# Optimization experiments

Hardware: AMD Instinct MI355X
Metric: run time of the kernel (lower is better)

## Reference

```python
import jax, jax.numpy as jnp
from jax import lax
import numpy as np

H_SIZE = 1024      # max(hidden_size_list)
EXPAND = 2
INTER = EXPAND * H_SIZE            # 2048 intermediate size
NHEADS = 32                        # max(num_heads_list)
HEAD_DIM = INTER // NHEADS         # 64
NSTATE = 128                       # ssm state size
NGROUPS = 1
KCONV = 4                          # conv kernel
CHUNK = 256                        # chunk size for SSD scan
EPS = 1e-5                         # layer_norm_epsilon
CONV_DIM = INTER + 2 * NGROUPS * NSTATE        # 2304
PROJ_DIM = 2 * INTER + 2 * NGROUPS * NSTATE + NHEADS  # 4352


def setup_inputs() -> dict:
    key = jax.random.key(0)
    ks = jax.random.split(key, 9)
    B, S = 2, 4096
    return {
        "hidden_states": jax.random.normal(ks[0], (B, S, H_SIZE), jnp.float32),
        "in_proj_w": jax.random.normal(ks[1], (PROJ_DIM, H_SIZE), jnp.float32) * 0.02,
        "conv_w": jax.random.normal(ks[2], (CONV_DIM, 1, KCONV), jnp.float32) * 0.2,
        "conv_b": jax.random.normal(ks[3], (CONV_DIM,), jnp.float32) * 0.02,
        "dt_bias": jax.random.normal(ks[4], (NHEADS,), jnp.float32) * 0.1,
        "A_log": jax.random.uniform(ks[5], (NHEADS,), jnp.float32, 0.0, 1.0),
        "D": jax.random.normal(ks[6], (NHEADS,), jnp.float32),
        "norm_w": jnp.ones((INTER,), jnp.float32) + 0.01 * jax.random.normal(ks[7], (INTER,), jnp.float32),
        "out_proj_w": jax.random.normal(ks[8], (H_SIZE, INTER), jnp.float32) * 0.02,
    }


def _segsum(a):
    # a: [B,H,C,L] -> lower-triangular segment sums [B,H,C,L,L]
    L = a.shape[-1]
    cs = jnp.cumsum(a, axis=-1)
    ss = cs[..., :, None] - cs[..., None, :]
    mask = jnp.tril(jnp.ones((L, L), dtype=bool))
    return jnp.where(mask, ss, -jnp.inf)


def reference(hidden_states, in_proj_w, conv_w, conv_b, dt_bias, A_log, D, norm_w, out_proj_w):
    B, S, _ = hidden_states.shape
    proj = hidden_states @ in_proj_w.T                       # [B,S,4352]
    gate = proj[..., :INTER]                                 # [B,S,2048]
    hBC = proj[..., INTER:INTER + CONV_DIM]                  # [B,S,2304]
    dt = proj[..., INTER + CONV_DIM:]                        # [B,S,H]

    # causal depthwise conv1d + SiLU
    xc_ = jnp.transpose(hBC, (0, 2, 1))                      # [B,C,S]
    xc_ = lax.conv_general_dilated(xc_, conv_w, (1,), [(KCONV - 1, 0)],
                                   dimension_numbers=('NCH', 'OIH', 'NCH'),
                                   feature_group_count=CONV_DIM)
    xc_ = jax.nn.silu(xc_ + conv_b[None, :, None])
    hBC = jnp.transpose(xc_, (0, 2, 1))                      # [B,S,2304]

    h = hBC[..., :INTER]
    Bm = hBC[..., INTER:INTER + NGROUPS * NSTATE]
    Cm = hBC[..., INTER + NGROUPS * NSTATE:]

    dt = jax.nn.softplus(dt + dt_bias)                       # [B,S,H]
    dt = jnp.clip(dt, 0.0, None)                             # time_step_limit (0, inf)
    A = -jnp.exp(A_log)                                      # [H]

    NC = S // CHUNK
    xh = h.reshape(B, NC, CHUNK, NHEADS, HEAD_DIM)
    Bh = jnp.repeat(Bm.reshape(B, NC, CHUNK, NGROUPS, NSTATE), NHEADS // NGROUPS, axis=3)
    Ch = jnp.repeat(Cm.reshape(B, NC, CHUNK, NGROUPS, NSTATE), NHEADS // NGROUPS, axis=3)
    dtc = dt.reshape(B, NC, CHUNK, NHEADS)

    a = jnp.transpose(dtc * A, (0, 3, 1, 2))                 # [B,H,NC,L]
    A_cum = jnp.cumsum(a, axis=-1)                           # [B,H,NC,L]
    Lmat = jnp.exp(_segsum(a))                               # [B,H,NC,L,L]
    xdt = xh * dtc[..., None]                                # [B,NC,L,H,P]

    # intra-chunk (diagonal block) output
    Yd = jnp.einsum('bclhn,bcshn,bhcls,bcshp->bclhp', Ch, Bh, Lmat, xdt)

    # per-chunk final states
    decay = jnp.exp(A_cum[..., -1:] - A_cum)                 # [B,H,NC,L]
    states = jnp.einsum('bclhn,bhcl,bclhp->bchpn', Bh, decay, xdt)  # [B,NC,H,P,N]

    # inter-chunk recurrence over chunks
    g = jnp.exp(A_cum[..., -1])                              # [B,H,NC]
    def step(carry, inp):
        s_c, g_c = inp
        return carry * g_c[..., None, None] + s_c, carry
    _, prev = lax.scan(step, jnp.zeros((B, NHEADS, HEAD_DIM, NSTATE), states.dtype),
                       (jnp.moveaxis(states, 1, 0), jnp.moveaxis(g, 2, 0)))
    prev = jnp.moveaxis(prev, 0, 1)                          # [B,NC,H,P,N] state entering each chunk

    Yo = jnp.einsum('bclhn,bchpn,bhcl->bclhp', Ch, prev, jnp.exp(A_cum))

    y = (Yd + Yo + D[None, None, None, :, None] * xh).reshape(B, S, INTER)

    # gated RMSNorm (fp32 internally)
    yf = y.astype(jnp.float32) * jax.nn.silu(gate.astype(jnp.float32))
    var = jnp.mean(yf * yf, axis=-1, keepdims=True)
    y = norm_w * (yf * lax.rsqrt(var + EPS))

    return y @ out_proj_w.T
```

## Files before the change

### kernel.cpp

```cpp
#include <hip/hip_runtime.h>
#include <hip/hip_bf16.h>
#include <math.h>

#define H_SIZE   1024
#define INTER    2048
#define NHEADS   32
#define HEAD_DIM 64
#define NSTATE   128
#define KCONV    4
#define CHUNK    256
#define CONV_DIM (INTER + 2*NSTATE)
#define CIN_DIM  (CONV_DIM + NHEADS)
#define PROJ_DIM (2*INTER + 2*NSTATE + NHEADS)
#define BATCH    2
#define SEQ      4096
#define NC       (SEQ/CHUNK)
#define EPS_F    1e-5f

typedef __attribute__((ext_vector_type(8))) short bf16x8;
typedef __attribute__((ext_vector_type(4))) float f32x4;
typedef unsigned short ushort_t;

__device__ __forceinline__ ushort_t f2bf(float x) {
  unsigned u = __float_as_uint(x);
  u += 0x7fffu + ((u >> 16) & 1u);
  return (ushort_t)(u >> 16);
}
__device__ __forceinline__ float bf2f(ushort_t h) {
  return __uint_as_float((unsigned)h << 16);
}

__global__ __launch_bounds__(256) void convert_hl_kernel(
    const float* __restrict__ x, ushort_t* __restrict__ hi,
    ushort_t* __restrict__ lo, int n4) {
  int idx = blockIdx.x * 256 + threadIdx.x;
  int stride = gridDim.x * 256;
  for (int i = idx; i < n4; i += stride) {
    const float* p = x + (size_t)i * 4;
    float v0 = p[0], v1 = p[1], v2 = p[2], v3 = p[3];
    ushort_t h0 = f2bf(v0), h1 = f2bf(v1), h2 = f2bf(v2), h3 = f2bf(v3);
    ushort_t l0 = f2bf(v0 - bf2f(h0));
    ushort_t l1 = f2bf(v1 - bf2f(h1));
    ushort_t l2 = f2bf(v2 - bf2f(h2));
    ushort_t l3 = f2bf(v3 - bf2f(h3));
    *(uint2*)(hi + (size_t)i * 4) =
        make_uint2((unsigned)h0 | ((unsigned)h1 << 16), (unsigned)h2 | ((unsigned)h3 << 16));
    *(uint2*)(lo + (size_t)i * 4) =
        make_uint2((unsigned)l0 | ((unsigned)l1 << 16), (unsigned)l2 | ((unsigned)l3 << 16));
  }
}

__global__ __launch_bounds__(256) void convert_bc_kernel(
    const float* __restrict__ hbc, ushort_t* __restrict__ Bph,
    ushort_t* __restrict__ Bpl, ushort_t* __restrict__ Cph,
    ushort_t* __restrict__ Cpl) {
  const int n4 = (BATCH*SEQ) * 64;
  int idx = blockIdx.x * 256 + threadIdx.x;
  int stride = gridDim.x * 256;
  for (int i = idx; i < n4; i += stride) {
    int row = i >> 6;
    int c4 = (i & 63) * 4;
    float4 v = *(const float4*)(hbc + (size_t)row*CONV_DIM + INTER + c4);
    ushort_t h0 = f2bf(v.x), h1 = f2bf(v.y), h2 = f2bf(v.z), h3 = f2bf(v.w);
    ushort_t l0 = f2bf(v.x - bf2f(h0)), l1 = f2bf(v.y - bf2f(h1));
    ushort_t l2 = f2bf(v.z - bf2f(h2)), l3 = f2bf(v.w - bf2f(h3));
    uint2 hp = make_uint2((unsigned)h0 | ((unsigned)h1 << 16), (unsigned)h2 | ((unsigned)h3 << 16));
    uint2 lp = make_uint2((unsigned)l0 | ((unsigned)l1 << 16), (unsigned)l2 | ((unsigned)l3 << 16));
    if (c4 < 128) {
      *(uint2*)(Bph + (size_t)row*128 + c4) = hp;
      *(uint2*)(Bpl + (size_t)row*128 + c4) = lp;
    } else {
      *(uint2*)(Cph + (size_t)row*128 + (c4 - 128)) = hp;
      *(uint2*)(Cpl + (size_t)row*128 + (c4 - 128)) = lp;
    }
  }
}

#define LROW 40
template<int PLANES>
__global__ __launch_bounds__(256) void gemm_hl_mfma_kernel(
    const ushort_t* __restrict__ Ahi, const ushort_t* __restrict__ Alo,
    const ushort_t* __restrict__ Whi, const ushort_t* __restrict__ Wlo,
    float* __restrict__ C, int M, int N, int K, int nx) {
  __shared__ __align__(16) ushort_t Ah[128*LROW];
  __shared__ __align__(16) ushort_t Al[(PLANES==3) ? 128*LROW : 8];
  __shared__ __align__(16) ushort_t Wh[128*LROW], Wl[128*LROW];
  const int tid = threadIdx.x;
  const int lane = tid & 63, wid = tid >> 6;
  const int wr = wid >> 1, wc = wid & 1;
  const int fr = lane & 15, fg = lane >> 4;

  const int cpx = gridDim.x >> 3;
  const int logical = (blockIdx.x & 7) * cpx + (blockIdx.x >> 3);
  const int grp = logical / (nx * 4);
  const int rem = logical - grp * (nx * 4);
  const int bx = rem >> 2;
  const int by = grp * 4 + (rem & 3);
  const int m0 = by * 128, n0 = bx * 128;

  const int r0 = tid >> 2;
  const int kseg = (tid & 3) * 8;
  const int r1 = r0 + 64;
  const size_t a0 = (size_t)(m0 + r0) * K + kseg;
  const size_t a1 = (size_t)(m0 + r1) * K + kseg;
  const size_t w0 = (size_t)(n0 + r0) * K + kseg;
  const size_t w1 = (size_t)(n0 + r1) * K + kseg;
  const bool wv0 = (n0 + r0) < N, wv1 = (n0 + r1) < N;

  bf16x8 gA0, gA1, gAl0, gAl1, gW0, gW1, gWl0, gWl1;
  const bf16x8 z8 = {};
  f32x4 acc[4][4] = {};

  auto glod = [&](int k0) {
    gA0  = *(const bf16x8*)(Ahi + a0 + k0);
    gA1  = *(const bf16x8*)(Ahi + a1 + k0);
    if constexpr (PLANES == 3) {
      gAl0 = *(const bf16x8*)(Alo + a0 + k0);
      gAl1 = *(const bf16x8*)(Alo + a1 + k0);
    }
    gW0  = wv0 ? *(const bf16x8*)(Whi + w0 + k0) : z8;
    gW1  = wv1 ? *(const bf16x8*)(Whi + w1 + k0) : z8;
    gWl0 = wv0 ? *(const bf16x8*)(Wlo + w0 + k0) : z8;
    gWl1 = wv1 ? *(const bf16x8*)(Wlo + w1 + k0) : z8;
  };

  glod(0);
  for (int k0 = 0; k0 < K; k0 += 32) {
    __syncthreads();
    *(bf16x8*)&Ah[r0*LROW + kseg] = gA0;
    *(bf16x8*)&Ah[r1*LROW + kseg] = gA1;
    if constexpr (PLANES == 3) {
      *(bf16x8*)&Al[r0*LROW + kseg] = gAl0;
      *(bf16x8*)&Al[r1*LROW + kseg] = gAl1;
    }
    *(bf16x8*)&Wh[r0*LROW + kseg] = gW0;
    *(bf16x8*)&Wh[r1*LROW + kseg] = gW1;
    *(bf16x8*)&Wl[r0*LROW + kseg] = gWl0;
    *(bf16x8*)&Wl[r1*LROW + kseg] = gWl1;
    __syncthreads();
    if (k0 + 32 < K) glod(k0 + 32);

    bf16x8 wh[4], wl[4];
#pragma unroll
    for (int nf = 0; nf < 4; ++nf) {
      int off = (wc*64 + nf*16 + fr) * LROW + 8*fg;
      wh[nf] = *(const bf16x8*)&Wh[off];
      wl[nf] = *(const bf16x8*)&Wl[off];
    }
#pragma unroll
    for (int mf = 0; mf < 4; ++mf) {
      int aoff = (wr*64 + mf*16 + fr) * LROW + 8*fg;
      bf16x8 ah = *(const bf16x8*)&Ah[aoff];
      bf16x8 al;
      if constexpr (PLANES == 3) al = *(const bf16x8*)&Al[aoff];
#pragma unroll
      for (int nf = 0; nf < 4; ++nf) {
        acc[mf][nf] = __builtin_amdgcn_mfma_f32_16x16x32_bf16(ah, wh[nf], acc[mf][nf], 0, 0, 0);
        acc[mf][nf] = __builtin_amdgcn_mfma_f32_16x16x32_bf16(ah, wl[nf], acc[mf][nf], 0, 0, 0);
        if constexpr (PLANES == 3)
          acc[mf][nf] = __builtin_amdgcn_mfma_f32_16x16x32_bf16(al, wh[nf], acc[mf][nf], 0, 0, 0);
      }
    }
  }

#pragma unroll
  for (int mf = 0; mf < 4; ++mf)
#pragma unroll
    for (int nf = 0; nf < 4; ++nf) {
      int col = n0 + wc*64 + nf*16 + fr;
      if (col < N) {
        size_t base = (size_t)(m0 + wr*64 + mf*16 + fg*4) * N + col;
        f32x4 v = acc[mf][nf];
        C[base]               = v[0];
        C[base + (size_t)N]   = v[1];
        C[base + 2*(size_t)N] = v[2];
        C[base + 3*(size_t)N] = v[3];
      }
    }
}

__global__ __launch_bounds__(256) void conv_kernel(
    const float* __restrict__ cin, const float* __restrict__ cw,
    const float* __restrict__ cb, const float* __restrict__ dtb,
    float* __restrict__ hbc, float* __restrict__ dtp) {
  const int bs = blockIdx.x;
  const int b = bs / SEQ, s = bs % SEQ;
  const int tid = threadIdx.x;
  const float* base = cin + (size_t)b * SEQ * CIN_DIM;
  for (int c = tid; c < CONV_DIM; c += 256) {
    float acc = cb[c];
#pragma unroll
    for (int k = 0; k < KCONV; ++k) {
      int sp = s - (KCONV-1) + k;
      if (sp >= 0) acc = fmaf(cw[c*KCONV + k], base[(size_t)sp * CIN_DIM + c], acc);
    }
    acc = acc / (1.f + expf(-acc));
    hbc[(size_t)bs * CONV_DIM + c] = acc;
  }
  if (tid < NHEADS) {
    float d = cin[(size_t)bs * CIN_DIM + CONV_DIM + tid] + dtb[tid];
    d = (d > 20.f) ? d : log1pf(expf(d));
    dtp[(size_t)bs * NHEADS + tid] = d;
  }
}

__global__ __launch_bounds__(256) void cumsum_kernel(
    const float* __restrict__ dtp, const float* __restrict__ A_log,
    float* __restrict__ acum, float* __restrict__ gch) {
  const int c = blockIdx.x, h = blockIdx.y, b = blockIdx.z;
  const int tid = threadIdx.x;
  __shared__ float sm[CHUNK];
  const float A = -expf(A_log[h]);
  const int s = c * CHUNK + tid;
  float a = dtp[(size_t)(b*SEQ + s)*NHEADS + h] * A;
  sm[tid] = a;
  __syncthreads();
  for (int off = 1; off < CHUNK; off <<= 1) {
    float v = 0.f;
    if (tid >= off) v = sm[tid - off];
    __syncthreads();
    sm[tid] += v;
    __syncthreads();
  }
  float ac = sm[tid];
  acum[((size_t)(b*NHEADS + h)*NC + c)*CHUNK + tid] = ac;
  if (tid == CHUNK-1) gch[(size_t)(b*NHEADS + h)*NC + c] = expf(ac);
}

#define CBROW 136
#define XROW2 72
__global__ __launch_bounds__(256) void yd_mfma_kernel(
    const ushort_t* __restrict__ Bph, const ushort_t* __restrict__ Bpl,
    const ushort_t* __restrict__ Cph, const ushort_t* __restrict__ Cpl,
    const float* __restrict__ hbc, const float* __restrict__ acum,
    const float* __restrict__ dtp, const float* __restrict__ Dv,
    float* __restrict__ y) {
  __shared__ __align__(16) ushort_t BhS[64*CBROW], BlS[64*CBROW];
  __shared__ __align__(16) ushort_t XhS[64*XROW2], XlS[64*XROW2];
  __shared__ __align__(16) ushort_t GhS[4][16*XROW2], GlS[4][16*XROW2];
  __shared__ float acLs[64], acSs[64];

  const int h = blockIdx.x;
  const int c = blockIdx.y >> 2, lt = blockIdx.y & 3;
  const int b = blockIdx.z;
  const int tid = threadIdx.x;
  const int lane = tid & 63, w = tid >> 6;
  const int fr = lane & 15, fg = lane >> 4;

  const size_t seqbase = (size_t)(b*SEQ + c*CHUNK);
  const size_t acbase  = ((size_t)(b*NHEADS + h)*NC + c)*CHUNK;

  bf16x8 cfh[4], cfl[4];
  {
    const size_t cg = (seqbase + lt*64 + w*16 + fr) * 128;
#pragma unroll
    for (int ks = 0; ks < 4; ++ks) {
      int ko = ks*32 + fg*8;
      cfh[ks] = *(const bf16x8*)(Cph + cg + ko);
      cfl[ks] = *(const bf16x8*)(Cpl + cg + ko);
    }
  }
  if (tid < 64) acLs[tid] = acum[acbase + lt*64 + tid];

  f32x4 acc[4] = {};

  for (int st = 0; st <= lt; ++st) {
    __syncthreads();
    {
      const size_t g0 = (seqbase + st*64) * 128;
#pragma unroll
      for (int i = 0; i < 4; ++i) {
        int f = tid + 256*i; int r = f >> 4; int k8 = (f & 15) * 8;
        *(bf16x8*)&BhS[r*CBROW + k8] = *(const bf16x8*)(Bph + g0 + (size_t)r*128 + k8);
        *(bf16x8*)&BlS[r*CBROW + k8] = *(const bf16x8*)(Bpl + g0 + (size_t)r*128 + k8);
      }
    }
#pragma unroll
    for (int i = 0; i < 4; ++i) {
      int f = tid + 256*i; int s = f >> 4; int p0 = (f & 15) * 4;
      size_t row = seqbase + st*64 + s;
      float dtv = dtp[row*NHEADS + h];
      float4 xv = *(const float4*)(hbc + row*CONV_DIM + h*HEAD_DIM + p0);
      float vals[4] = {xv.x*dtv, xv.y*dtv, xv.z*dtv, xv.w*dtv};
#pragma unroll
      for (int j = 0; j < 4; ++j) {
        int p = p0 + j;
        int sw = s ^ (((p >> 2) & 7) << 3);
        ushort_t hh = f2bf(vals[j]);
        ushort_t ll = f2bf(vals[j] - bf2f(hh));
        XhS[p*XROW2 + sw] = hh;
        XlS[p*XROW2 + sw] = ll;
      }
    }
    if (tid < 64) acSs[tid] = acum[acbase + st*64 + tid];
    __syncthreads();

    f32x4 g[4] = {};
#pragma unroll
    for (int ks = 0; ks < 4; ++ks) {
      const int ko = ks*32 + fg*8;
#pragma unroll
      for (int nf = 0; nf < 4; ++nf) {
        const int rb = (nf*16 + fr) * CBROW + ko;
        bf16x8 bh = *(const bf16x8*)&BhS[rb];
        bf16x8 bl = *(const bf16x8*)&BlS[rb];
        g[nf] = __builtin_amdgcn_mfma_f32_16x16x32_bf16(cfh[ks], bh, g[nf], 0, 0, 0);
        g[nf] = __builtin_amdgcn_mfma_f32_16x16x32_bf16(cfh[ks], bl, g[nf], 0, 0, 0);
        g[nf] = __builtin_amdgcn_mfma_f32_16x16x32_bf16(cfl[ks], bh, g[nf], 0, 0, 0);
      }
    }
    {
      const bool full = (st < lt);
#pragma unroll
      for (int nf = 0; nf < 4; ++nf) {
        int sl = nf*16 + fr;
        float aS = acSs[sl];
#pragma unroll
        for (int r = 0; r < 4; ++r) {
          int ll = w*16 + fg*4 + r;
          float v = 0.f;
          if (full || ll >= sl) v = g[nf][r] * __expf(acLs[ll] - aS);
          ushort_t hh = f2bf(v);
          ushort_t lo2 = f2bf(v - bf2f(hh));
          GhS[w][(fg*4 + r)*XROW2 + sl] = hh;
          GlS[w][(fg*4 + r)*XROW2 + sl] = lo2;
        }
      }
    }
    __syncthreads();
#pragma unroll
    for (int ks = 0; ks < 2; ++ks) {
      const int ko = ks*32 + fg*8;
      bf16x8 gh = *(const bf16x8*)&GhS[w][fr*XROW2 + ko];
      bf16x8 gl = *(const bf16x8*)&GlS[w][fr*XROW2 + ko];
#pragma unroll
      for (int nf = 0; nf < 4; ++nf) {
        int p = nf*16 + fr;
        int kb = ko ^ (((p >> 2) & 7) << 3);
        bf16x8 xh = *(const bf16x8*)&XhS[p*XROW2 + kb];
        bf16x8 xl = *(const bf16x8*)&XlS[p*XROW2 + kb];
        acc[nf] = __builtin_amdgcn_mfma_f32_16x16x32_bf16(gh, xh, acc[nf], 0, 0, 0);
        acc[nf] = __builtin_amdgcn_mfma_f32_16x16x32_bf16(gh, xl, acc[nf], 0, 0, 0);
        acc[nf] = __builtin_amdgcn_mfma_f32_16x16x32_bf16(gl, xh, acc[nf], 0, 0, 0);
      }
    }
  }

  const float Dh = Dv[h];
#pragma unroll
  for (int nf = 0; nf < 4; ++nf) {
    int p = nf*16 + fr;
#pragma unroll
    for (int r = 0; r < 4; ++r) {
      size_t row = seqbase + lt*64 + w*16 + fg*4 + r;
      float xval = hbc[row*CONV_DIM + h*HEAD_DIM + p];
      y[row*INTER + h*HEAD_DIM + p] = acc[nf][r] + Dh * xval;
    }
  }
}

#define SXROW 72
__global__ __launch_bounds__(256) void states_mfma_kernel(
    const ushort_t* __restrict__ Bph, const ushort_t* __restrict__ Bpl,
    const float* __restrict__ hbc, const float* __restrict__ acum,
    const float* __restrict__ dtp, float* __restrict__ states) {
  __shared__ __align__(16) ushort_t XhS[64*SXROW], XlS[64*SXROW];
  __shared__ __align__(16) ushort_t BhS[128*SXROW], BlS[128*SXROW];
  const int h = blockIdx.x, c = blockIdx.y, b = blockIdx.z;
  const int tid = threadIdx.x;
  const int lane = tid & 63, w = tid >> 6;
  const int fr = lane & 15, fg = lane >> 4;
  const size_t seqbase = (size_t)(b*SEQ + c*CHUNK);
  const size_t acbase  = ((size_t)(b*NHEADS + h)*NC + c)*CHUNK;
  const float aclast = acum[acbase + CHUNK - 1];
  f32x4 acc[8] = {};

  for (int lt = 0; lt < 4; ++lt) {
    __syncthreads();
#pragma unroll
    for (int i = 0; i < 4; ++i) {
      int f = tid + 256*i; int l = f >> 4; int p0 = (f & 15) * 4;
      size_t row = seqbase + lt*64 + l;
      float mult = dtp[row*NHEADS + h] * __expf(aclast - acum[acbase + lt*64 + l]);
      float4 xv = *(const float4*)(hbc + row*CONV_DIM + h*HEAD_DIM + p0);
      float vals[4] = {xv.x*mult, xv.y*mult, xv.z*mult, xv.w*mult};
#pragma unroll
      for (int j = 0; j < 4; ++j) {
        int p = p0 + j;
        int sw = l ^ (((p >> 2) & 7) << 3);
        ushort_t hh = f2bf(vals[j]);
        XhS[p*SXROW + sw] = hh;
        XlS[p*SXROW + sw] = f2bf(vals[j] - bf2f(hh));
      }
    }
#pragma unroll
    for (int i = 0; i < 4; ++i) {
      int f = tid + 256*i; int l = f >> 4; int n8 = (f & 15) * 8;
      size_t g0 = (seqbase + lt*64 + l) * 128 + n8;
      bf16x8 bh = *(const bf16x8*)(Bph + g0);
      bf16x8 bl = *(const bf16x8*)(Bpl + g0);
#pragma unroll
      for (int j = 0; j < 8; ++j) {
        int n = n8 + j;
        int sw = l ^ (((n >> 2) & 7) << 3);
        BhS[n*SXROW + sw] = (ushort_t)bh[j];
        BlS[n*SXROW + sw] = (ushort_t)bl[j];
      }
    }
    __syncthreads();
#pragma unroll
    for (int ks = 0; ks < 2; ++ks) {
      const int ko = ks*32 + fg*8;
      const int pa = w*16 + fr;
      const int ka = ko ^ (((pa >> 2) & 7) << 3);
      bf16x8 ah = *(const bf16x8*)&XhS[pa*SXROW + ka];
      bf16x8 al = *(const bf16x8*)&XlS[pa*SXROW + ka];
#pragma unroll
      for (int nf = 0; nf < 8; ++nf) {
        const int nb = nf*16 + fr;
        const int kb = ko ^ (((nb >> 2) & 7) << 3);
        bf16x8 bh = *(const bf16x8*)&BhS[nb*SXROW + kb];
        bf16x8 bl = *(const bf16x8*)&BlS[nb*SXROW + kb];
        acc[nf] = __builtin_amdgcn_mfma_f32_16x16x32_bf16(ah, bh, acc[nf], 0, 0, 0);
        acc[nf] = __builtin_amdgcn_mfma_f32_16x16x32_bf16(ah, bl, acc[nf], 0, 0, 0);
        acc[nf] = __builtin_amdgcn_mfma_f32_16x16x32_bf16(al, bh, acc[nf], 0, 0, 0);
      }
    }
  }
  float* sp = states + ((size_t)(b*NC + c)*NHEADS + h)*HEAD_DIM*NSTATE;
#pragma unroll
  for (int nf = 0; nf < 8; ++nf) {
    int n = nf*16 + fr;
#pragma unroll
    for (int r = 0; r < 4; ++r) {
      int p = w*16 + fg*4 + r;
      sp[(size_t)p*NSTATE + n] = acc[nf][r];
    }
  }
}

__global__ __launch_bounds__(1024) void scan_kernel(
    float* __restrict__ st, const float* __restrict__ g) {
  const int bh = blockIdx.x;
  const int b = bh >> 5, h = bh & 31;
  const int tid = threadIdx.x;
  float carry[8];
#pragma unroll
  for (int i = 0; i < 8; ++i) carry[i] = 0.f;
  for (int c = 0; c < NC; ++c) {
    const float gc = g[(size_t)(b*NHEADS + h)*NC + c];
    float* base = st + ((size_t)(b*NC + c)*NHEADS + h)*HEAD_DIM*NSTATE;
    ushort_t* ub = (ushort_t*)base;
    float sv[8];
#pragma unroll
    for (int i = 0; i < 8; ++i) sv[i] = base[i*1024 + tid];
    __syncthreads();
#pragma unroll
    for (int i = 0; i < 8; ++i) {
      int e = i*1024 + tid;
      ushort_t hh = f2bf(carry[i]);
      ub[e]        = hh;
      ub[8192 + e] = f2bf(carry[i] - bf2f(hh));
      carry[i] = fmaf(carry[i], gc, sv[i]);
    }
  }
}

#define PROW 136
__global__ __launch_bounds__(256) void yo_mfma_kernel(
    const ushort_t* __restrict__ Cph, const ushort_t* __restrict__ Cpl,
    const ushort_t* __restrict__ stp, const float* __restrict__ acum,
    float* __restrict__ y) {
  __shared__ __align__(16) ushort_t PhS[64*PROW], PlS[64*PROW];
  const int h = blockIdx.x, c = blockIdx.y, b = blockIdx.z;
  const int tid = threadIdx.x;
  const int lane = tid & 63, w = tid >> 6;
  const int fr = lane & 15, fg = lane >> 4;
  const size_t seqbase = (size_t)(b*SEQ + c*CHUNK);
  const size_t acbase  = ((size_t)(b*NHEADS + h)*NC + c)*CHUNK;

  const ushort_t* pb = stp + ((size_t)(b*NC + c)*NHEADS + h) * (size_t)(2*HEAD_DIM*NSTATE);
#pragma unroll
  for (int i = 0; i < 4; ++i) {
    int f = tid + 256*i; int r = f >> 4; int k8 = (f & 15) * 8;
    *(bf16x8*)&PhS[r*PROW + k8] = *(const bf16x8*)(pb + (size_t)r*128 + k8);
    *(bf16x8*)&PlS[r*PROW + k8] = *(const bf16x8*)(pb + 8192 + (size_t)r*128 + k8);
  }
  __syncthreads();

  for (int lt = 0; lt < 4; ++lt) {
    const size_t cg = (seqbase + lt*64 + w*16 + fr) * 128;
    f32x4 acc[4] = {};
#pragma unroll
    for (int ks = 0; ks < 4; ++ks) {
      int ko = ks*32 + fg*8;
      bf16x8 ah = *(const bf16x8*)(Cph + cg + ko);
      bf16x8 al = *(const bf16x8*)(Cpl + cg + ko);
#pragma unroll
      for (int nf = 0; nf < 4; ++nf) {
        const int rb = (nf*16 + fr) * PROW + ko;
        bf16x8 bh = *(const bf16x8*)&PhS[rb];
        bf16x8 bl = *(const bf16x8*)&PlS[rb];
        acc[nf] = __builtin_amdgcn_mfma_f32_16x16x32_bf16(ah, bh, acc[nf], 0, 0, 0);
        acc[nf] = __builtin_amdgcn_mfma_f32_16x16x32_bf16(ah, bl, acc[nf], 0, 0, 0);
        acc[nf] = __builtin_amdgcn_mfma_f32_16x16x32_bf16(al, bh, acc[nf], 0, 0, 0);
      }
    }
#pragma unroll
    for (int r = 0; r < 4; ++r) {
      int lrow = lt*64 + w*16 + fg*4 + r;
      float e = __expf(acum[acbase + lrow]);
      float* yrow = y + (seqbase + lrow)*INTER + h*HEAD_DIM;
#pragma unroll
      for (int nf = 0; nf < 4; ++nf) {
        int p = nf*16 + fr;
        yrow[p] += e * acc[nf][r];
      }
    }
  }
}

__global__ __launch_bounds__(256) void rms_kernel(
    const float* __restrict__ y, const float* __restrict__ gate,
    const float* __restrict__ norm_w, ushort_t* __restrict__ yh) {
  const int bs = blockIdx.x;
  const int tid = threadIdx.x;
  const float* yrow = y + (size_t)bs * INTER;
  const float* grow = gate + (size_t)bs * INTER;
  float yf[8];
  float ss = 0.f;
#pragma unroll
  for (int i = 0; i < 8; ++i) {
    int c = tid + i*256;
    float v = yrow[c];
    float gt = grow[c];
    float f = v * (gt / (1.f + expf(-gt)));
    yf[i] = f;
    ss += f*f;
  }
#pragma unroll
  for (int off = 32; off >= 1; off >>= 1) ss += __shfl_xor(ss, off, 64);
  __shared__ float red[4];
  if ((tid & 63) == 0) red[tid >> 6] = ss;
  __syncthreads();
  float total = red[0] + red[1] + red[2] + red[3];
  float sc = rsqrtf(total * (1.f/INTER) + EPS_F);
#pragma unroll
  for (int i = 0; i < 8; ++i) {
    int c = tid + i*256;
    yh[(size_t)bs*INTER + c] = f2bf(norm_w[c] * yf[i] * sc);
  }
}

__global__ void zero_kernel(float* p, size_t n) {
  size_t i = (size_t)blockIdx.x * blockDim.x + threadIdx.x;
  if (i < n) p[i] = 0.f;
}

extern "C" void kernel_launch(void* const* d_in, const int* in_sizes, int n_in,
                              void* d_out, int out_size, void* d_ws, size_t ws_size,
                              hipStream_t stream) {
  const float* hidden = (const float*)d_in[0];
  const float* in_w   = (const float*)d_in[1];
  const float* conv_w = (const float*)d_in[2];
  const float* conv_b = (const float*)d_in[3];
  const float* dt_b   = (const float*)d_in[4];
  const float* A_log  = (const float*)d_in[5];
  const float* Dv     = (const float*)d_in[6];
  const float* norm_w = (const float*)d_in[7];
  const float* out_w  = (const float*)d_in[8];
  float* out = (float*)d_out;

  const int M = BATCH*SEQ;

  const size_t sz_cin  = (size_t)M * CIN_DIM;
  const size_t sz_hbc  = (size_t)M * CONV_DIM;
  const size_t sz_dtp  = (size_t)M * NHEADS;
  const size_t sz_acum = (size_t)BATCH*NHEADS*NC*CHUNK;
  const size_t sz_gch  = (size_t)BATCH*NHEADS*NC;
  const size_t sz_R    = (size_t)BATCH*NC*NHEADS*HEAD_DIM*NSTATE;
  const size_t need = (sz_cin + sz_hbc + sz_dtp + sz_acum + sz_gch + sz_R) * sizeof(float);

  if (ws_size < need) {
    size_t n = (size_t)out_size;
    zero_kernel<<<(unsigned)((n + 255) / 256), 256, 0, stream>>>(out, n);
    return;
  }

  float* ws = (float*)d_ws;
  size_t o = 0;
  float* cin  = ws + o; o += sz_cin;
  float* hbc  = ws + o; o += sz_hbc;
  float* dtp  = ws + o; o += sz_dtp;
  float* acum = ws + o; o += sz_acum;
  float* gch  = ws + o; o += sz_gch;
  float* R    = ws + o; o += sz_R;

  float* y    = cin;
  float* gate = hbc;
  float* st   = R;

  ushort_t* hidhi = (ushort_t*)R;
  ushort_t* hidlo = hidhi + (size_t)M * H_SIZE;
  ushort_t* yhR   = (ushort_t*)R;
  ushort_t* wplh  = (ushort_t*)hbc;

  ushort_t* wscr = (ushort_t*)out;
  const size_t MP = (size_t)M * 128;
  ushort_t* bcp  = (ushort_t*)((char*)d_out + (size_t)(16u << 20));
  ushort_t* Bph = bcp;
  ushort_t* Bpl = bcp + MP;
  ushort_t* Cph = bcp + 2*MP;
  ushort_t* Cpl = bcp + 3*MP;

  {
    int nA4 = (M * H_SIZE) / 4;
    int nW  = CIN_DIM * H_SIZE;
    int nx = (CIN_DIM + 127) / 128;
    convert_hl_kernel<<<2048, 256, 0, stream>>>(hidden, hidhi, hidlo, nA4);
    convert_hl_kernel<<<2048, 256, 0, stream>>>(in_w + (size_t)INTER*H_SIZE, wscr, wscr + nW, nW/4);
    gemm_hl_mfma_kernel<3><<<nx * (M/128), 256, 0, stream>>>(
        hidhi, hidlo, wscr, wscr + nW, cin, M, CIN_DIM, H_SIZE, nx);
  }
  conv_kernel<<<dim3(M), 256, 0, stream>>>(cin, conv_w, conv_b, dt_b, hbc, dtp);
  convert_bc_kernel<<<2048, 256, 0, stream>>>(hbc, Bph, Bpl, Cph, Cpl);
  cumsum_kernel<<<dim3(NC, NHEADS, BATCH), 256, 0, stream>>>(dtp, A_log, acum, gch);
  yd_mfma_kernel<<<dim3(NHEADS, NC*4, BATCH), 256, 0, stream>>>(
      Bph, Bpl, Cph, Cpl, hbc, acum, dtp, Dv, y);
  states_mfma_kernel<<<dim3(NHEADS, NC, BATCH), 256, 0, stream>>>(
      Bph, Bpl, hbc, acum, dtp, st);
  scan_kernel<<<dim3(BATCH*NHEADS), 1024, 0, stream>>>(st, gch);
  yo_mfma_kernel<<<dim3(NHEADS, NC, BATCH), 256, 0, stream>>>(
      Cph, Cpl, (const ushort_t*)st, acum, y);
  {
    int nA4 = (M * H_SIZE) / 4;
    int nW  = INTER * H_SIZE;
    int nx = INTER / 128;
    convert_hl_kernel<<<2048, 256, 0, stream>>>(hidden, hidhi, hidlo, nA4);
    convert_hl_kernel<<<2048, 256, 0, stream>>>(in_w, wscr, wscr + nW, nW/4);
    gemm_hl_mfma_kernel<2><<<nx * (M/128), 256, 0, stream>>>(
        hidhi, hidlo, wscr, wscr + nW, gate, M, INTER, H_SIZE, nx);
  }
  rms_kernel<<<dim3(M), 256, 0, stream>>>(y, gate, norm_w, yhR);
  {
    int nW  = H_SIZE * INTER;
    convert_hl_kernel<<<2048, 256, 0, stream>>>(out_w, wplh, wplh + nW, nW/4);
    int nx = H_SIZE / 128;
    gemm_hl_mfma_kernel<2><<<nx * (M/128), 256, 0, stream>>>(
        yhR, yhR, wplh, wplh + nW, out, M, H_SIZE, INTER, nx);
  }
}
```

Before: 735.0 us.

## Split in-proj GEMM by precision, fuse conv with B/C conversion and dt into cumsum

The projection GEMM for the conv/dt columns is split in two. The first 2048 x-channel columns run with 2-plane (hi*hi + hi*lo) MFMA, and only the B/C/dt columns keep 3-plane precision. A leading-dimension parameter is added so both halves write into the shared output. The conv kernel is rewritten to process 8 rows per thread with a register sliding window and to emit the bf16 hi/lo B/C planes directly, which removes the separate convert_bc pass; softplus of dt moves into the cumsum kernel. This cuts MFMA work and memory traffic, at the risk of reduced precision on the x channels.

Measured after the change: 659.6 us. 1.11x faster.

```diff
diff --git a/kernel.cpp b/kernel.cpp
--- a/kernel.cpp
+++ b/kernel.cpp
@@ -50,38 +50,12 @@
   }
 }
 
-__global__ __launch_bounds__(256) void convert_bc_kernel(
-    const float* __restrict__ hbc, ushort_t* __restrict__ Bph,
-    ushort_t* __restrict__ Bpl, ushort_t* __restrict__ Cph,
-    ushort_t* __restrict__ Cpl) {
-  const int n4 = (BATCH*SEQ) * 64;
-  int idx = blockIdx.x * 256 + threadIdx.x;
-  int stride = gridDim.x * 256;
-  for (int i = idx; i < n4; i += stride) {
-    int row = i >> 6;
-    int c4 = (i & 63) * 4;
-    float4 v = *(const float4*)(hbc + (size_t)row*CONV_DIM + INTER + c4);
-    ushort_t h0 = f2bf(v.x), h1 = f2bf(v.y), h2 = f2bf(v.z), h3 = f2bf(v.w);
-    ushort_t l0 = f2bf(v.x - bf2f(h0)), l1 = f2bf(v.y - bf2f(h1));
-    ushort_t l2 = f2bf(v.z - bf2f(h2)), l3 = f2bf(v.w - bf2f(h3));
-    uint2 hp = make_uint2((unsigned)h0 | ((unsigned)h1 << 16), (unsigned)h2 | ((unsigned)h3 << 16));
-    uint2 lp = make_uint2((unsigned)l0 | ((unsigned)l1 << 16), (unsigned)l2 | ((unsigned)l3 << 16));
-    if (c4 < 128) {
-      *(uint2*)(Bph + (size_t)row*128 + c4) = hp;
-      *(uint2*)(Bpl + (size_t)row*128 + c4) = lp;
-    } else {
-      *(uint2*)(Cph + (size_t)row*128 + (c4 - 128)) = hp;
-      *(uint2*)(Cpl + (size_t)row*128 + (c4 - 128)) = lp;
-    }
-  }
-}
-
 #define LROW 40
 template<int PLANES>
 __global__ __launch_bounds__(256) void gemm_hl_mfma_kernel(
     const ushort_t* __restrict__ Ahi, const ushort_t* __restrict__ Alo,
     const ushort_t* __restrict__ Whi, const ushort_t* __restrict__ Wlo,
-    float* __restrict__ C, int M, int N, int K, int nx) {
+    float* __restrict__ C, int M, int N, int K, int nx, int ldc) {
   __shared__ __align__(16) ushort_t Ah[128*LROW];
   __shared__ __align__(16) ushort_t Al[(PLANES==3) ? 128*LROW : 8];
   __shared__ __align__(16) ushort_t Wh[128*LROW], Wl[128*LROW];
@@ -169,50 +143,64 @@
     for (int nf = 0; nf < 4; ++nf) {
       int col = n0 + wc*64 + nf*16 + fr;
       if (col < N) {
-        size_t base = (size_t)(m0 + wr*64 + mf*16 + fg*4) * N + col;
+        size_t base = (size_t)(m0 + wr*64 + mf*16 + fg*4) * ldc + col;
         f32x4 v = acc[mf][nf];
-        C[base]               = v[0];
-        C[base + (size_t)N]   = v[1];
-        C[base + 2*(size_t)N] = v[2];
-        C[base + 3*(size_t)N] = v[3];
-      }
-    }
-}
-
-__global__ __launch_bounds__(256) void conv_kernel(
+        C[base]                 = v[0];
+        C[base + (size_t)ldc]   = v[1];
+        C[base + 2*(size_t)ldc] = v[2];
+        C[base + 3*(size_t)ldc] = v[3];
+      }
+    }
+}
+
+__global__ __launch_bounds__(256) void conv2_kernel(
     const float* __restrict__ cin, const float* __restrict__ cw,
-    const float* __restrict__ cb, const float* __restrict__ dtb,
-    float* __restrict__ hbc, float* __restrict__ dtp) {
-  const int bs = blockIdx.x;
-  const int b = bs / SEQ, s = bs % SEQ;
-  const int tid = threadIdx.x;
-  const float* base = cin + (size_t)b * SEQ * CIN_DIM;
-  for (int c = tid; c < CONV_DIM; c += 256) {
-    float acc = cb[c];
-#pragma unroll
-    for (int k = 0; k < KCONV; ++k) {
-      int sp = s - (KCONV-1) + k;
-      if (sp >= 0) acc = fmaf(cw[c*KCONV + k], base[(size_t)sp * CIN_DIM + c], acc);
-    }
+    const float* __restrict__ cb, float* __restrict__ hbc,
+    ushort_t* __restrict__ Bph, ushort_t* __restrict__ Bpl,
+    ushort_t* __restrict__ Cph, ushort_t* __restrict__ Cpl) {
+  const int c = blockIdx.x * 256 + threadIdx.x;
+  const int r0 = blockIdx.y * 8;
+  const int s0 = r0 & (SEQ - 1);
+  const float w0 = cw[c*KCONV+0], w1 = cw[c*KCONV+1];
+  const float w2 = cw[c*KCONV+2], w3 = cw[c*KCONV+3];
+  const float bias = cb[c];
+  const float* cp = cin + (size_t)r0 * CIN_DIM + c;
+  float xm3 = (s0 > 0) ? cp[-3*CIN_DIM] : 0.f;
+  float xm2 = (s0 > 0) ? cp[-2*CIN_DIM] : 0.f;
+  float xm1 = (s0 > 0) ? cp[-1*CIN_DIM] : 0.f;
+#pragma unroll
+  for (int i = 0; i < 8; ++i) {
+    float x0 = cp[(size_t)i * CIN_DIM];
+    float acc = fmaf(w0, xm3, fmaf(w1, xm2, fmaf(w2, xm1, fmaf(w3, x0, bias))));
     acc = acc / (1.f + expf(-acc));
-    hbc[(size_t)bs * CONV_DIM + c] = acc;
-  }
-  if (tid < NHEADS) {
-    float d = cin[(size_t)bs * CIN_DIM + CONV_DIM + tid] + dtb[tid];
-    d = (d > 20.f) ? d : log1pf(expf(d));
-    dtp[(size_t)bs * NHEADS + tid] = d;
+    size_t row = (size_t)(r0 + i);
+    if (c < INTER) {
+      hbc[row*CONV_DIM + c] = acc;
+    } else {
+      ushort_t hh = f2bf(acc);
+      ushort_t ll = f2bf(acc - bf2f(hh));
+      int cc = c - INTER;
+      if (cc < NSTATE) { Bph[row*NSTATE + cc] = hh; Bpl[row*NSTATE + cc] = ll; }
+      else { Cph[row*NSTATE + (cc-NSTATE)] = hh; Cpl[row*NSTATE + (cc-NSTATE)] = ll; }
+    }
+    xm3 = xm2; xm2 = xm1; xm1 = x0;
   }
 }
 
 __global__ __launch_bounds__(256) void cumsum_kernel(
-    const float* __restrict__ dtp, const float* __restrict__ A_log,
+    const float* __restrict__ cin, const float* __restrict__ A_log,
+    const float* __restrict__ dtb, float* __restrict__ dtp,
     float* __restrict__ acum, float* __restrict__ gch) {
   const int c = blockIdx.x, h = blockIdx.y, b = blockIdx.z;
   const int tid = threadIdx.x;
   __shared__ float sm[CHUNK];
   const float A = -expf(A_log[h]);
   const int s = c * CHUNK + tid;
-  float a = dtp[(size_t)(b*SEQ + s)*NHEADS + h] * A;
+  const size_t row = (size_t)(b*SEQ + s);
+  float draw = cin[row*CIN_DIM + CONV_DIM + h] + dtb[h];
+  float d = (draw > 20.f) ? draw : log1pf(expf(draw));
+  dtp[row*NHEADS + h] = d;
+  float a = d * A;
   sm[tid] = a;
   __syncthreads();
   for (int off = 1; off < CHUNK; off <<= 1) {
@@ -616,15 +604,18 @@
   {
     int nA4 = (M * H_SIZE) / 4;
     int nW  = CIN_DIM * H_SIZE;
-    int nx = (CIN_DIM + 127) / 128;
     convert_hl_kernel<<<2048, 256, 0, stream>>>(hidden, hidhi, hidlo, nA4);
     convert_hl_kernel<<<2048, 256, 0, stream>>>(in_w + (size_t)INTER*H_SIZE, wscr, wscr + nW, nW/4);
-    gemm_hl_mfma_kernel<3><<<nx * (M/128), 256, 0, stream>>>(
-        hidhi, hidlo, wscr, wscr + nW, cin, M, CIN_DIM, H_SIZE, nx);
-  }
-  conv_kernel<<<dim3(M), 256, 0, stream>>>(cin, conv_w, conv_b, dt_b, hbc, dtp);
-  convert_bc_kernel<<<2048, 256, 0, stream>>>(hbc, Bph, Bpl, Cph, Cpl);
-  cumsum_kernel<<<dim3(NC, NHEADS, BATCH), 256, 0, stream>>>(dtp, A_log, acum, gch);
+    gemm_hl_mfma_kernel<2><<<16 * (M/128), 256, 0, stream>>>(
+        hidhi, hidlo, wscr, wscr + nW, cin, M, 2048, H_SIZE, 16, CIN_DIM);
+    gemm_hl_mfma_kernel<3><<<3 * (M/128), 256, 0, stream>>>(
+        hidhi, hidlo, wscr + (size_t)2048*H_SIZE, wscr + nW + (size_t)2048*H_SIZE,
+        cin + 2048, M, 288, H_SIZE, 3, CIN_DIM);
+  }
+  conv2_kernel<<<dim3(CONV_DIM/256, M/8), 256, 0, stream>>>(
+      cin, conv_w, conv_b, hbc, Bph, Bpl, Cph, Cpl);
+  cumsum_kernel<<<dim3(NC, NHEADS, BATCH), 256, 0, stream>>>(
+      cin, A_log, dt_b, dtp, acum, gch);
   yd_mfma_kernel<<<dim3(NHEADS, NC*4, BATCH), 256, 0, stream>>>(
       Bph, Bpl, Cph, Cpl, hbc, acum, dtp, Dv, y);
   states_mfma_kernel<<<dim3(NHEADS, NC, BATCH), 256, 0, stream>>>(
@@ -635,18 +626,16 @@
   {
     int nA4 = (M * H_SIZE) / 4;
     int nW  = INTER * H_SIZE;
-    int nx = INTER / 128;
     convert_hl_kernel<<<2048, 256, 0, stream>>>(hidden, hidhi, hidlo, nA4);
     convert_hl_kernel<<<2048, 256, 0, stream>>>(in_w, wscr, wscr + nW, nW/4);
-    gemm_hl_mfma_kernel<2><<<nx * (M/128), 256, 0, stream>>>(
-        hidhi, hidlo, wscr, wscr + nW, gate, M, INTER, H_SIZE, nx);
+    gemm_hl_mfma_kernel<2><<<16 * (M/128), 256, 0, stream>>>(
+        hidhi, hidlo, wscr, wscr + nW, gate, M, INTER, H_SIZE, 16, INTER);
   }
   rms_kernel<<<dim3(M), 256, 0, stream>>>(y, gate, norm_w, yhR);
   {
     int nW  = H_SIZE * INTER;
     convert_hl_kernel<<<2048, 256, 0, stream>>>(out_w, wplh, wplh + nW, nW/4);
-    int nx = H_SIZE / 128;
-    gemm_hl_mfma_kernel<2><<<nx * (M/128), 256, 0, stream>>>(
-        yhR, yhR, wplh, wplh + nW, out, M, H_SIZE, INTER, nx);
-  }
-}
+    gemm_hl_mfma_kernel<2><<<8 * (M/128), 256, 0, stream>>>(
+        yhR, yhR, wplh, wplh + nW, out, M, H_SIZE, INTER, 8, H_SIZE);
+  }
+}
```
